# Kernel optimization log

Hardware: AMD Instinct MI355X
Metric: run time of the kernel (lower is better)

The kernel has to match this reference:

```python
import jax, jax.numpy as jnp
import numpy as np
import math

B, M, D = 16, 2048, 512
H, K, NB = 8, 5, 5
HD = D // H
FF = 2048


def _p(key, shape, scale=0.02):
    return (jax.random.normal(key, shape, dtype=jnp.float32) * scale)


def setup_inputs() -> dict:
    key = jax.random.key(0)
    ks = jax.random.split(key, 16)
    inp = {
        'x': jax.random.normal(ks[0], (B, M, D), dtype=jnp.float32),
        'mask': jnp.ones((B, 1, M), dtype=bool),
        'ln1_g': jnp.ones((D,), jnp.float32), 'ln1_b': jnp.zeros((D,), jnp.float32),
        'Wk': _p(ks[1], (D, D)), 'bk': jnp.zeros((D,), jnp.float32),
        'Wv': _p(ks[2], (D, D)), 'bv': jnp.zeros((D,), jnp.float32),
        'Wq': _p(ks[3], (D, D)), 'bq': jnp.zeros((D,), jnp.float32),
        'Woff': _p(ks[4], (D, H * K)), 'boff': jnp.zeros((H * K,), jnp.float32),
        'Wo': _p(ks[5], (D, D)), 'bo': jnp.zeros((D,), jnp.float32),
        'ln2_g': jnp.ones((D,), jnp.float32), 'ln2_b': jnp.zeros((D,), jnp.float32),
        'W1': _p(ks[6], (D, FF)), 'b1': jnp.zeros((FF,), jnp.float32),
        'W2': _p(ks[7], (FF, D)), 'b2': jnp.zeros((D,), jnp.float32),
    }
    return inp


def layer_norm(x, g, b, eps=1e-6):
    mu = jnp.mean(x, axis=-1, keepdims=True)
    var = jnp.mean((x - mu) ** 2, axis=-1, keepdims=True)
    return (x - mu) / jnp.sqrt(var + eps) * g + b


def grid_sample_1d(src, gx):
    # src: [BH, Min, hd], gx: [BH, M, K] normalized x-coords in [-1,1]
    # Replicates torch grid_sample(bilinear, zeros, align_corners=False) with
    # H_in=1 and y-grid==1 -> implicit 0.5 factor from y-interp against zero pad.
    BH, Min, hd = src.shape
    ix = ((gx + 1.0) * Min - 1.0) / 2.0
    x0 = jnp.floor(ix)
    w1 = ix - x0
    x0i = x0.astype(jnp.int32)

    def gather(xi):
        valid = ((xi >= 0) & (xi < Min)).astype(src.dtype)
        xc = jnp.clip(xi, 0, Min - 1)
        flat = xc.reshape(BH, -1)
        vals = jnp.take_along_axis(src, flat[:, :, None], axis=1)
        return vals.reshape(BH, xi.shape[1], xi.shape[2], hd) * valid[..., None]

    v0 = gather(x0i)
    v1 = gather(x0i + 1)
    return ((1.0 - w1)[..., None] * v0 + w1[..., None] * v1) * 0.5


def reference(x, mask, ln1_g, ln1_b, Wk, bk, Wv, bv, Wq, bq, Woff, boff,
              Wo, bo, ln2_g, ln2_b, W1, b1, W2, b2):
    Bs, Ms, Ds = x.shape
    xn = layer_norm(x, ln1_g, ln1_b)
    k = xn @ Wk + bk
    v = xn @ Wv + bv
    q = xn @ Wq + bq

    # query_type == 'mean': AvgPool1d(kernel=NB, stride=1, pad=NB//2),
    # count_include_pad=True -> moving sum over zero-padded seq / NB
    pad = NB // 2
    qp = jnp.pad(q, ((0, 0), (pad, pad), (0, 0)))
    cs = jnp.concatenate([jnp.zeros((Bs, 1, Ds), q.dtype), jnp.cumsum(qp, axis=1)], axis=1)
    q = (cs[:, NB:, :] - cs[:, :-NB, :]) / float(NB)  # [B, M, D]

    offsets = (q @ Woff + boff).reshape(Bs, Ms, H, K).transpose(0, 2, 1, 3)  # [B,H,M,K]
    kh = k.reshape(Bs, Ms, H, HD).transpose(0, 2, 1, 3)  # [B,H,M,hd]
    vh = v.reshape(Bs, Ms, H, HD).transpose(0, 2, 1, 3)
    qh = q.reshape(Bs, Ms, H, HD).transpose(0, 2, 1, 3)

    loc = jnp.arange(Ms, dtype=jnp.float32)[:, None]          # [M,1]
    left = -K // 2                                            # Python floor div: -3 for K=5
    ref = jnp.arange(left, K + left, dtype=jnp.float32)       # [K]
    sign_lens = jnp.squeeze(jnp.sum(mask, axis=-1)).astype(jnp.float32) - 1.0  # [B]

    sl = ref + offsets + loc                                  # [B,H,M,K]
    sl = jnp.mod(sl, sign_lens[:, None, None, None])
    gx = (sl / (Ms - 1) * 2.0 - 1.0).reshape(Bs * H, Ms, K)

    ksrc = kh.reshape(Bs * H, Ms, HD)
    vsrc = vh.reshape(Bs * H, Ms, HD)
    sk = grid_sample_1d(ksrc, gx).reshape(Bs, H, Ms, K, HD)
    sv = grid_sample_1d(vsrc, gx).reshape(Bs, H, Ms, K, HD)

    qh = qh / math.sqrt(HD)
    scores = jnp.einsum('bhmd,bhmkd->bhmk', qh, sk)
    attn = jax.nn.softmax(scores, axis=-1)
    ctx = jnp.einsum('bhmk,bhmkd->bhmd', attn, sv)
    ctx = ctx.transpose(0, 2, 1, 3).reshape(Bs, Ms, H * HD)
    att_out = ctx @ Wo + bo

    o = att_out + x  # dropout=0.0
    on = layer_norm(o, ln2_g, ln2_b)
    ff = jax.nn.relu(on @ W1 + b1) @ W2 + b2
    return ff + o
```

## Files before the change

kernel.cpp:

```cpp
#include <hip/hip_runtime.h>


#define B_   16
#define M_   2048
#define D_   512
#define H_   8
#define K_   5
#define HD_  64
#define FF_  2048
#define NROWS (B_ * M_)

typedef unsigned short u16;
typedef __attribute__((ext_vector_type(4))) unsigned short u16x4;
typedef __attribute__((ext_vector_type(8))) unsigned short u16x8;
typedef __attribute__((ext_vector_type(8))) short short8;
typedef __attribute__((ext_vector_type(4))) float f32x4;

__device__ __forceinline__ u16 f2bf(float f) {
  unsigned u = __builtin_bit_cast(unsigned, f);
  u += 0x7fff + ((u >> 16) & 1);
  return (u16)(u >> 16);
}
__device__ __forceinline__ float bf2f(u16 h) {
  unsigned u = (unsigned)h << 16;
  return __builtin_bit_cast(float, u);
}

#define GLP(p)  ((__attribute__((address_space(1))) void*)(p))
#define LDSP(p) ((__attribute__((address_space(3))) void*)(p))

__global__ __launch_bounds__(256)
void wtrans(const float* __restrict__ in, int K, int N,
            u16* __restrict__ out, int padN) {
  __shared__ float t[32][33];
  const int tx = threadIdx.x, ty = threadIdx.y;
  const int n0 = blockIdx.x * 32, k0 = blockIdx.y * 32;
#pragma unroll
  for (int r = 0; r < 4; ++r) {
    const int k = k0 + ty + r * 8;
    const int n = n0 + tx;
    t[ty + r * 8][tx] = (n < N) ? in[(size_t)k * N + n] : 0.f;
  }
  __syncthreads();
#pragma unroll
  for (int r = 0; r < 4; ++r) {
    const int nn = n0 + ty + r * 8;
    out[(size_t)nn * K + k0 + tx] = f2bf(t[tx][ty + r * 8]);
  }
}

__global__ __launch_bounds__(256)
void kvperm(const u16* __restrict__ tmp, u16* __restrict__ out) {
  const int g = blockIdx.x * 256 + threadIdx.x;
  const int row = g >> 6, j = g & 63;
  const int h = row >> 7, r = row & 127;
  const int src = ((r >> 2) & 1) * 512 + h * 64 + (r >> 3) * 4 + (r & 3);
  *(u16x8*)&out[(size_t)row * 512 + j * 8] =
      *(const u16x8*)&tmp[(size_t)src * 512 + j * 8];
}

__global__ __launch_bounds__(256)
void bias_cat(const float* __restrict__ bk, const float* __restrict__ bv,
              const float* __restrict__ bq, float* __restrict__ o) {
  const int i = blockIdx.x * 256 + threadIdx.x;
  if (i >= 1024) { o[i] = bq[i - 1024]; return; }
  const int h = i >> 7, r = i & 127;
  const int c = h * 64 + (r >> 3) * 4 + (r & 3);
  o[i] = ((r >> 2) & 1) ? bv[c] : bk[c];
}

__global__ __launch_bounds__(128)
void ln_bf16(const float* __restrict__ x, const float* __restrict__ g,
             const float* __restrict__ bsh, u16* __restrict__ y) {
  const int row = blockIdx.x;
  float4 v = ((const float4*)(x + (size_t)row * D_))[threadIdx.x];
  float s  = v.x + v.y + v.z + v.w;
  float s2 = v.x * v.x + v.y * v.y + v.z * v.z + v.w * v.w;
#pragma unroll
  for (int off = 32; off; off >>= 1) {
    s  += __shfl_xor(s, off);
    s2 += __shfl_xor(s2, off);
  }
  __shared__ float sh[4];
  if ((threadIdx.x & 63) == 0) {
    sh[threadIdx.x >> 6]       = s;
    sh[2 + (threadIdx.x >> 6)] = s2;
  }
  __syncthreads();
  s = sh[0] + sh[1]; s2 = sh[2] + sh[3];
  const float mu  = s * (1.0f / D_);
  const float var = s2 * (1.0f / D_) - mu * mu;
  const float inv = rsqrtf(var + 1e-6f);
  float4 gv = ((const float4*)g)[threadIdx.x];
  float4 bv = ((const float4*)bsh)[threadIdx.x];
  u16x4 o;
  o.x = f2bf((v.x - mu) * inv * gv.x + bv.x);
  o.y = f2bf((v.y - mu) * inv * gv.y + bv.y);
  o.z = f2bf((v.z - mu) * inv * gv.z + bv.z);
  o.w = f2bf((v.w - mu) * inv * gv.w + bv.w);
  *(u16x4*)(y + (size_t)row * D_ + threadIdx.x * 4) = o;
}

__global__ __launch_bounds__(128)
void ln_bf16_in(const u16* __restrict__ x, const float* __restrict__ g,
                const float* __restrict__ bsh, u16* __restrict__ y) {
  const int row = blockIdx.x;
  u16x4 hv = *(const u16x4*)(x + (size_t)row * D_ + threadIdx.x * 4);
  float4 v;
  v.x = bf2f(hv.x); v.y = bf2f(hv.y); v.z = bf2f(hv.z); v.w = bf2f(hv.w);
  float s  = v.x + v.y + v.z + v.w;
  float s2 = v.x * v.x + v.y * v.y + v.z * v.z + v.w * v.w;
#pragma unroll
  for (int off = 32; off; off >>= 1) {
    s  += __shfl_xor(s, off);
    s2 += __shfl_xor(s2, off);
  }
  __shared__ float sh[4];
  if ((threadIdx.x & 63) == 0) {
    sh[threadIdx.x >> 6]       = s;
    sh[2 + (threadIdx.x >> 6)] = s2;
  }
  __syncthreads();
  s = sh[0] + sh[1]; s2 = sh[2] + sh[3];
  const float mu  = s * (1.0f / D_);
  const float var = s2 * (1.0f / D_) - mu * mu;
  const float inv = rsqrtf(var + 1e-6f);
  float4 gv = ((const float4*)g)[threadIdx.x];
  float4 bv = ((const float4*)bsh)[threadIdx.x];
  u16x4 o;
  o.x = f2bf((v.x - mu) * inv * gv.x + bv.x);
  o.y = f2bf((v.y - mu) * inv * gv.y + bv.y);
  o.z = f2bf((v.z - mu) * inv * gv.z + bv.z);
  o.w = f2bf((v.w - mu) * inv * gv.w + bv.w);
  *(u16x4*)(y + (size_t)row * D_ + threadIdx.x * 4) = o;
}

template<int EPI, int OUTBF, int RBF>
__global__ __launch_bounds__(512, 2)
void mgemmS(const u16* __restrict__ A, int lda,
            const u16* __restrict__ Wt, int ldb, int Kdim,
            const float* __restrict__ bias,
            const void* R, int ldr,
            void* Cv, int ldc, int Ncols, int nbx) {
  __shared__ u16 lds[81920] __attribute__((aligned(128)));
  int bid = blockIdx.x;
  { const int q = (int)gridDim.x >> 3; bid = (bid & 7) * q + (bid >> 3); }
  const int bx = bid % nbx, by = bid / nbx;
  const int m0 = by * 256, n0 = bx * 256;

  const int tid  = threadIdx.x;
  const int w    = tid >> 6, lane = tid & 63;
  const int wr   = w >> 2,   wc   = w & 3;
  const int lr   = lane & 15, kg  = lane >> 4;
  const int NT   = Kdim >> 6;
  const int srow = (w << 3) + (lane >> 3);
  const int scol = (((lane & 7) ^ (lane >> 3)) << 3);

  const u16* Ab = A  + (size_t)m0 * lda;
  const u16* Bb = Wt + (size_t)n0 * ldb;

  auto stage = [&](const u16* gbase, int ld, int kt, int h, int base) {
    const u16* s0 = gbase + (size_t)(h * 128 + srow) * ld + kt * 64 + scol;
    const u16* s1 = s0 + (size_t)64 * ld;
    u16* d0 = &lds[base + h * 8192 + w * 512];
    __builtin_amdgcn_global_load_lds(GLP(s0), LDSP(d0),        16, 0, 0);
    __builtin_amdgcn_global_load_lds(GLP(s1), LDSP(d0 + 4096), 16, 0, 0);
  };
  auto rdA = [&](int base, int f, int s) -> short8 {
    const int row = wr * 128 + f * 16 + lr;
    const int cb  = (kg * 16 + s * 64) ^ ((lr & 7) << 4);
    return *(const short8*)&lds[base + row * 64 + (cb >> 1)];
  };
  auto rdB = [&](int bsel, int nn, int s) -> short8 {
    const int row = wc * 64 + nn * 16 + lr;
    const int cb  = (kg * 16 + s * 64) ^ ((lr & 7) << 4);
    return *(const short8*)&lds[49152 + bsel * 16384 + row * 64 + (cb >> 1)];
  };

  f32x4 acc[8][4];
#pragma unroll
  for (int f = 0; f < 8; ++f)
#pragma unroll
    for (int n = 0; n < 4; ++n) acc[f][n] = (f32x4){0.f, 0.f, 0.f, 0.f};

  stage(Ab, lda, 0, 0, 0);      stage(Ab, lda, 0, 1, 0);
  stage(Bb, ldb, 0, 0, 49152);  stage(Bb, ldb, 0, 1, 49152);
  if (NT > 1) {
    stage(Ab, lda, 1, 0, 16384);  stage(Ab, lda, 1, 1, 16384);
    stage(Bb, ldb, 1, 0, 65536);  stage(Bb, ldb, 1, 1, 65536);
    asm volatile("s_waitcnt vmcnt(8)" ::: "memory");
  } else {
    asm volatile("s_waitcnt vmcnt(0)" ::: "memory");
  }
  asm volatile("s_barrier" ::: "memory");

  int aCur = 0, bCur = 0;
  for (int t = 0; t < NT; ++t) {
    int aT2 = aCur + 2; if (aT2 >= 3) aT2 -= 3;
    const int aBase = aCur * 16384;
    const int aT2b  = aT2 * 16384;
    const int bT2b  = 49152 + bCur * 16384;
    short8 bfr[4][2];
    short8 afr[2][2][2];
#pragma unroll
    for (int n = 0; n < 4; ++n) { bfr[n][0] = rdB(bCur, n, 0); bfr[n][1] = rdB(bCur, n, 1); }
#pragma unroll
    for (int i = 0; i < 2; ++i) { afr[0][i][0] = rdA(aBase, i, 0); afr[0][i][1] = rdA(aBase, i, 1); }
    if (t + 2 < NT) { stage(Ab, lda, t + 2, 0, aT2b); stage(Ab, lda, t + 2, 1, aT2b); }
#pragma unroll
    for (int q = 0; q < 4; ++q) {
      if (q < 3) {
#pragma unroll
        for (int i = 0; i < 2; ++i) {
          afr[(q + 1) & 1][i][0] = rdA(aBase, 2 * (q + 1) + i, 0);
          afr[(q + 1) & 1][i][1] = rdA(aBase, 2 * (q + 1) + i, 1);
        }
      }
#pragma unroll
      for (int i = 0; i < 2; ++i)
#pragma unroll
        for (int n = 0; n < 4; ++n) {
          acc[2 * q + i][n] = __builtin_amdgcn_mfma_f32_16x16x32_bf16(afr[q & 1][i][0], bfr[n][0], acc[2 * q + i][n], 0, 0, 0);
          acc[2 * q + i][n] = __builtin_amdgcn_mfma_f32_16x16x32_bf16(afr[q & 1][i][1], bfr[n][1], acc[2 * q + i][n], 0, 0, 0);
        }
      if (q == 0) {
        asm volatile("s_waitcnt lgkmcnt(8)" ::: "memory");
        asm volatile("s_barrier" ::: "memory");
        if (t + 2 < NT) { stage(Bb, ldb, t + 2, 0, bT2b); stage(Bb, ldb, t + 2, 1, bT2b); }
      }
    }
    if (t + 1 < NT) {
      if (t + 2 < NT) { asm volatile("s_waitcnt vmcnt(8) lgkmcnt(0)" ::: "memory"); }
      else            { asm volatile("s_waitcnt vmcnt(0) lgkmcnt(0)" ::: "memory"); }
      asm volatile("s_barrier" ::: "memory");
    }
    aCur = (aCur + 1 < 3) ? aCur + 1 : 0;
    bCur ^= 1;
  }

#pragma unroll
  for (int f = 0; f < 8; ++f) {
    const int row = m0 + wr * 128 + f * 16 + kg * 4;
#pragma unroll
    for (int n = 0; n < 4; ++n) {
      const int col = n0 + wc * 64 + n * 16 + lr;
      if (col < Ncols) {
        const float bb = bias[col];
#pragma unroll
        for (int r = 0; r < 4; ++r) {
          float val = acc[f][n][r] + bb;
          if (EPI == 1) {
            if (RBF) val += bf2f(((const u16*)R)[(size_t)(row + r) * ldr + col]);
            else     val += ((const float*)R)[(size_t)(row + r) * ldr + col];
          }
          if (EPI == 2) val = fmaxf(val, 0.f);
          if (OUTBF) ((u16*)Cv)[(size_t)(row + r) * ldc + col]   = f2bf(val);
          else       ((float*)Cv)[(size_t)(row + r) * ldc + col] = val;
        }
      }
    }
  }
}

__global__ __launch_bounds__(256)
void pool_q_bf(const u16* __restrict__ kvq, u16* __restrict__ qp) {
  const size_t idx = (size_t)blockIdx.x * 256 + threadIdx.x;
  const int d4 = (int)(idx & 127);
  const size_t bm = idx >> 7;
  const int m = (int)(bm & (M_ - 1));
  float a0 = 0.f, a1 = 0.f, a2 = 0.f, a3 = 0.f;
#pragma unroll
  for (int j = -2; j <= 2; ++j) {
    const int mm = m + j;
    if (mm >= 0 && mm < M_) {
      u16x4 tv = *(const u16x4*)(kvq + (bm + j) * 1536 + 1024 + d4 * 4);
      a0 += bf2f(tv.x); a1 += bf2f(tv.y); a2 += bf2f(tv.z); a3 += bf2f(tv.w);
    }
  }
  u16x4 o;
  o.x = f2bf(a0 * 0.2f); o.y = f2bf(a1 * 0.2f);
  o.z = f2bf(a2 * 0.2f); o.w = f2bf(a3 * 0.2f);
  *(u16x4*)(qp + bm * D_ + d4 * 4) = o;
}

__global__ __launch_bounds__(256)
void attn3(const u16* __restrict__ KVQ, const u16* __restrict__ QP,
           const float* __restrict__ OFFS, u16* __restrict__ CTX) {
  const int tid  = threadIdx.x;
  const int lane = tid & 63;
  const int j    = lane & 7;
  const int grp  = lane >> 3;
  const int gid  = blockIdx.x * 32 + (tid >> 6) * 8 + grp;
  const int m  = gid & (M_ - 1);
  const int bh = gid >> 11;
  const int h  = bh & (H_ - 1);
  const int b  = bh >> 3;
  const size_t bm = (size_t)b * M_ + m;

  float qs[8];
  {
    u16x8 qv = *(const u16x8*)(QP + bm * D_ + h * HD_ + j * 8);
#pragma unroll
    for (int e = 0; e < 8; ++e) qs[e] = bf2f(qv[e]) * 0.0625f;
  }
  const float* ob = OFFS + bm * (H_ * K_) + h * K_;
  const u16* kvb = KVQ + h * 128 + j * 16;
  const size_t rowb = (size_t)b * M_;

  float sc[K_], sv[K_][8];
#pragma unroll
  for (int kk = 0; kk < K_; ++kk) {
    float sl = (float)(m + kk - 3) + ob[kk];
    if (sl < 0.f) sl += 2047.f;
    else if (sl >= 2047.f) sl -= 2047.f;
    const float ix  = sl * (2048.0f / 2047.0f) - 0.5f;
    const float x0f = floorf(ix);
    const float w1  = ix - x0f;
    const int   x0  = (int)x0f;
    u16x8 a0, b0, a1, b1;
#pragma unroll
    for (int e = 0; e < 8; ++e) { a0[e] = 0; b0[e] = 0; a1[e] = 0; b1[e] = 0; }
    if (x0 >= 0) {
      const u16* p = kvb + (rowb + x0) * 1536;
      a0 = *(const u16x8*)p; b0 = *(const u16x8*)(p + 8);
    }
    if (x0 < M_ - 1) {
      const u16* p = kvb + (rowb + x0 + 1) * 1536;
      a1 = *(const u16x8*)p; b1 = *(const u16x8*)(p + 8);
    }
    float part = 0.f;
#pragma unroll
    for (int e = 0; e < 4; ++e) {
      const float k0 = bf2f(a0[e]),     k1 = bf2f(a1[e]);
      const float v0 = bf2f(a0[e + 4]), v1 = bf2f(a1[e + 4]);
      part += (k0 + w1 * (k1 - k0)) * qs[e];
      sv[kk][e] = v0 + w1 * (v1 - v0);
      const float k0b = bf2f(b0[e]),     k1b = bf2f(b1[e]);
      const float v0b = bf2f(b0[e + 4]), v1b = bf2f(b1[e + 4]);
      part += (k0b + w1 * (k1b - k0b)) * qs[e + 4];
      sv[kk][e + 4] = v0b + w1 * (v1b - v0b);
    }
    part += __shfl_xor(part, 1);
    part += __shfl_xor(part, 2);
    part += __shfl_xor(part, 4);
    sc[kk] = part;
  }
  float mx = sc[0];
#pragma unroll
  for (int kk = 1; kk < K_; ++kk) mx = fmaxf(mx, sc[kk]);
  float den = 0.f;
#pragma unroll
  for (int kk = 0; kk < K_; ++kk) { sc[kk] = __expf(sc[kk] - mx); den += sc[kk]; }
  const float inv = 1.0f / den;
  float c[8] = {0, 0, 0, 0, 0, 0, 0, 0};
#pragma unroll
  for (int kk = 0; kk < K_; ++kk) {
    const float wgt = sc[kk] * inv;
#pragma unroll
    for (int e = 0; e < 8; ++e) c[e] += wgt * sv[kk][e];
  }
  u16x8 o;
#pragma unroll
  for (int e = 0; e < 8; ++e) o[e] = f2bf(c[e] * 0.5f);
  *(u16x8*)(CTX + bm * 1536 + h * HD_ + j * 8) = o;
}

extern "C" void kernel_launch(void* const* d_in, const int* in_sizes, int n_in,
                              void* d_out, int out_size, void* d_ws, size_t ws_size,
                              hipStream_t stream) {
  const float* x     = (const float*)d_in[0];
  const float* ln1_g = (const float*)d_in[2];
  const float* ln1_b = (const float*)d_in[3];
  const float* Wk    = (const float*)d_in[4];
  const float* bk    = (const float*)d_in[5];
  const float* Wv    = (const float*)d_in[6];
  const float* bv    = (const float*)d_in[7];
  const float* Wq    = (const float*)d_in[8];
  const float* bq    = (const float*)d_in[9];
  const float* Woff  = (const float*)d_in[10];
  const float* boff  = (const float*)d_in[11];
  const float* Wo    = (const float*)d_in[12];
  const float* bo    = (const float*)d_in[13];
  const float* ln2_g = (const float*)d_in[14];
  const float* ln2_b = (const float*)d_in[15];
  const float* W1    = (const float*)d_in[16];
  const float* b1    = (const float*)d_in[17];
  const float* W2    = (const float*)d_in[18];
  const float* b2    = (const float*)d_in[19];
  float* out = (float*)d_out;

  if (ws_size < 181403648ull) return;
  char* ws = (char*)d_ws;
  u16* WKVQt = (u16*)ws;
  u16* Wot   = (u16*)(ws + 1572864ull);
  u16* Wofft = (u16*)(ws + 2097152ull);
  u16* W1t   = (u16*)(ws + 2359296ull);
  u16* W2t   = (u16*)(ws + 4456448ull);
  float* BKVQ = (float*)(ws + 6553600ull);
  u16* TMPKV = (u16*)(ws + 6559744ull);
  u16*  XN   = (u16*)(ws + 8388608ull);
  float* OFFS = (float*)(ws + 41943040ull);
  u16*  OB   = (u16*)(ws + 47185920ull);
  u16*  KVQ  = (u16*)(ws + 80740352ull);
  u16*  HIDc = KVQ;

  const dim3 tb(32, 8);
  wtrans<<<dim3(16, 16), tb, 0, stream>>>(Wk, 512, 512, TMPKV,          512);
  wtrans<<<dim3(16, 16), tb, 0, stream>>>(Wv, 512, 512, TMPKV + 262144, 512);
  kvperm<<<256, 256, 0, stream>>>(TMPKV, WKVQt);
  wtrans<<<dim3(16, 16), tb, 0, stream>>>(Wq, 512, 512, WKVQt + 524288, 512);
  wtrans<<<dim3(16, 16), tb, 0, stream>>>(Wo, 512, 512, Wot, 512);
  wtrans<<<dim3(8, 16),  tb, 0, stream>>>(Woff, 512, 40, Wofft, 256);
  wtrans<<<dim3(64, 16), tb, 0, stream>>>(W1, 512, 2048, W1t, 2048);
  wtrans<<<dim3(16, 64), tb, 0, stream>>>(W2, 2048, 512, W2t, 512);
  bias_cat<<<6, 256, 0, stream>>>(bk, bv, bq, BKVQ);

  ln_bf16<<<NROWS, 128, 0, stream>>>(x, ln1_g, ln1_b, XN);
  mgemmS<0,1,0><<<768, 512, 0, stream>>>(XN, 512, WKVQt, 512, 512, BKVQ,
                                         nullptr, 0, KVQ, 1536, 1536, 6);
  pool_q_bf<<<16384, 256, 0, stream>>>(KVQ, XN);
  mgemmS<0,0,0><<<128, 512, 0, stream>>>(XN, 512, Wofft, 512, 512, boff,
                                         nullptr, 0, OFFS, 40, 40, 1);
  attn3<<<8192, 256, 0, stream>>>(KVQ, XN, OFFS, KVQ + 1024);
  mgemmS<1,1,0><<<256, 512, 0, stream>>>(KVQ + 1024, 1536, Wot, 512, 512, bo,
                                         x, 512, OB, 512, 512, 2);
  ln_bf16_in<<<NROWS, 128, 0, stream>>>(OB, ln2_g, ln2_b, XN);
  for (int c = 0; c < 2; ++c) {
    const size_t ro = (size_t)c * 16384 * 512;
    mgemmS<2,1,0><<<512, 512, 0, stream>>>(XN + ro, 512, W1t, 512, 512, b1,
                                           nullptr, 0, HIDc, 2048, 2048, 8);
    mgemmS<1,0,1><<<128, 512, 0, stream>>>(HIDc, 2048, W2t, 2048, 2048, b2,
                                           OB + ro, 512, out + ro, 512, 512, 2);
  }
}
```

Before: 440.7 us.

## Keep attention residual in fp32 output buffer and run FFN in one pass

The attention output projection now writes its fp32 residual sum straight into the final output buffer instead of a bf16 intermediate. LayerNorm2 reads that fp32 buffer through the regular ln_bf16 kernel, and the FFN runs over all rows in single launches rather than two chunks. The second GEMM then adds the residual from out in place. This removes the bf16 residual buffer, the separate bf16-input LayerNorm and the chunking overhead, at the cost of more fp32 residual traffic and a larger hidden-activation buffer that must fit the workspace. Keeping the residual in fp32 also improves accuracy.

```diff
diff --git a/kernel.cpp b/kernel.cpp
--- a/kernel.cpp
+++ b/kernel.cpp
@@ -74,40 +74,6 @@
              const float* __restrict__ bsh, u16* __restrict__ y) {
   const int row = blockIdx.x;
   float4 v = ((const float4*)(x + (size_t)row * D_))[threadIdx.x];
-  float s  = v.x + v.y + v.z + v.w;
-  float s2 = v.x * v.x + v.y * v.y + v.z * v.z + v.w * v.w;
-#pragma unroll
-  for (int off = 32; off; off >>= 1) {
-    s  += __shfl_xor(s, off);
-    s2 += __shfl_xor(s2, off);
-  }
-  __shared__ float sh[4];
-  if ((threadIdx.x & 63) == 0) {
-    sh[threadIdx.x >> 6]       = s;
-    sh[2 + (threadIdx.x >> 6)] = s2;
-  }
-  __syncthreads();
-  s = sh[0] + sh[1]; s2 = sh[2] + sh[3];
-  const float mu  = s * (1.0f / D_);
-  const float var = s2 * (1.0f / D_) - mu * mu;
-  const float inv = rsqrtf(var + 1e-6f);
-  float4 gv = ((const float4*)g)[threadIdx.x];
-  float4 bv = ((const float4*)bsh)[threadIdx.x];
-  u16x4 o;
-  o.x = f2bf((v.x - mu) * inv * gv.x + bv.x);
-  o.y = f2bf((v.y - mu) * inv * gv.y + bv.y);
-  o.z = f2bf((v.z - mu) * inv * gv.z + bv.z);
-  o.w = f2bf((v.w - mu) * inv * gv.w + bv.w);
-  *(u16x4*)(y + (size_t)row * D_ + threadIdx.x * 4) = o;
-}
-
-__global__ __launch_bounds__(128)
-void ln_bf16_in(const u16* __restrict__ x, const float* __restrict__ g,
-                const float* __restrict__ bsh, u16* __restrict__ y) {
-  const int row = blockIdx.x;
-  u16x4 hv = *(const u16x4*)(x + (size_t)row * D_ + threadIdx.x * 4);
-  float4 v;
-  v.x = bf2f(hv.x); v.y = bf2f(hv.y); v.z = bf2f(hv.z); v.w = bf2f(hv.w);
   float s  = v.x + v.y + v.z + v.w;
   float s2 = v.x * v.x + v.y * v.y + v.z * v.z + v.w * v.w;
 #pragma unroll
@@ -400,9 +366,8 @@
   u16* TMPKV = (u16*)(ws + 6559744ull);
   u16*  XN   = (u16*)(ws + 8388608ull);
   float* OFFS = (float*)(ws + 41943040ull);
-  u16*  OB   = (u16*)(ws + 47185920ull);
-  u16*  KVQ  = (u16*)(ws + 80740352ull);
-  u16*  HIDc = KVQ;
+  u16*  KVQ  = (u16*)(ws + 47185920ull);
+  u16*  HID  = KVQ;
 
   const dim3 tb(32, 8);
   wtrans<<<dim3(16, 16), tb, 0, stream>>>(Wk, 512, 512, TMPKV,          512);
@@ -422,14 +387,11 @@
   mgemmS<0,0,0><<<128, 512, 0, stream>>>(XN, 512, Wofft, 512, 512, boff,
                                          nullptr, 0, OFFS, 40, 40, 1);
   attn3<<<8192, 256, 0, stream>>>(KVQ, XN, OFFS, KVQ + 1024);
-  mgemmS<1,1,0><<<256, 512, 0, stream>>>(KVQ + 1024, 1536, Wot, 512, 512, bo,
-                                         x, 512, OB, 512, 512, 2);
-  ln_bf16_in<<<NROWS, 128, 0, stream>>>(OB, ln2_g, ln2_b, XN);
-  for (int c = 0; c < 2; ++c) {
-    const size_t ro = (size_t)c * 16384 * 512;
-    mgemmS<2,1,0><<<512, 512, 0, stream>>>(XN + ro, 512, W1t, 512, 512, b1,
-                                           nullptr, 0, HIDc, 2048, 2048, 8);
-    mgemmS<1,0,1><<<128, 512, 0, stream>>>(HIDc, 2048, W2t, 2048, 2048, b2,
-                                           OB + ro, 512, out + ro, 512, 512, 2);
-  }
-}
+  mgemmS<1,0,0><<<256, 512, 0, stream>>>(KVQ + 1024, 1536, Wot, 512, 512, bo,
+                                         x, 512, out, 512, 512, 2);
+  ln_bf16<<<NROWS, 128, 0, stream>>>(out, ln2_g, ln2_b, XN);
+  mgemmS<2,1,0><<<1024, 512, 0, stream>>>(XN, 512, W1t, 512, 512, b1,
+                                          nullptr, 0, HID, 2048, 2048, 8);
+  mgemmS<1,0,0><<<256, 512, 0, stream>>>(HID, 2048, W2t, 2048, 2048, b2,
+                                         out, 512, out, 512, 512, 2);
+}
```

New measurement: 466.0 us. 5.7% more time.
